# Kernel tuning notes

Hardware: AMD Instinct MI355X
Metric: run time of the kernel (lower is better)

## Reference

```python
import jax, jax.numpy as jnp
import numpy as np


def setup_inputs() -> dict:
    key = jax.random.key(0)
    # [N, n, m]: batch, transform length (axis 1), columns
    x = jax.random.normal(key, (32, 1024, 512), dtype=jnp.float32)
    return {"x": x}


def reference(x):
    # Faithful port of idct_odd_case: IDCT-III via a length-2n complex IFFT
    # on a Hermitian-symmetric-style mirrored array, exactly as the TF code.
    N, n, m = x.shape
    k = jnp.arange(n, dtype=jnp.float32)
    # t[k] = sqrt(2n) * exp(i*pi*k/(2n)); t[0] scaled by extra sqrt(2)
    t = jnp.sqrt(2.0 * n) * jnp.exp(1j * k * (np.pi / (2.0 * n)))
    t = t.at[0].multiply(jnp.sqrt(2.0))
    W = t.astype(jnp.complex64)[None, :, None]           # [1, n, 1]
    xc = x.astype(jnp.complex64)
    yy_up = W * xc                                        # [N, n, m]
    # -i * W[1:n] * reverse(x[1:n]) along the transform axis
    yy_down = (-1j) * W[:, 1:, :] * xc[:, n - 1:0:-1, :]  # [N, n-1, m]
    yy_mid = jnp.zeros((N, 1, m), dtype=jnp.complex64)
    yy = jnp.concatenate([yy_up, yy_mid, yy_down], axis=1)  # [N, 2n, m]
    y = jnp.fft.ifft(yy, axis=1)                          # matlab_ifft: ifft on axis 1
    return jnp.real(y[:, :n, :]).astype(jnp.float32)
```

## Files before the change

### kernel.cpp

```cpp
#include <hip/hip_runtime.h>

typedef unsigned short u16;
typedef __attribute__((ext_vector_type(8))) __bf16 bf16x8;
typedef __attribute__((ext_vector_type(4))) float f32x4;

#define GLOAD_LDS16(g, l)                                                                     \
  __builtin_amdgcn_global_load_lds((const __attribute__((address_space(1))) unsigned int*)(g), \
                                   (__attribute__((address_space(3))) unsigned int*)(l), 16, 0, 0)

static __device__ __forceinline__ u16 f2bf(float f) {
  unsigned int u = __float_as_uint(f);
  u += 0x7fffu + ((u >> 16) & 1u);
  return (u16)(u >> 16);
}

#define BATCH 32
#define NN 1024
#define MM 512
#define KH 512

__global__ void fill_eo(u16* __restrict__ E, u16* __restrict__ O) {
  int idx = blockIdx.x * 256 + threadIdx.x;
  int j = idx >> 9;
  int p = idx & 511;
  int tj = 2 * j + 1;
  float ve;
  if (p == 0) {
    ve = 0.03125f;
  } else {
    int pe = (2 * p * tj) & 4095;
    ve = 0.04419417382415922f * cosf((float)pe * 1.5339807878856412e-3f);
  }
  int po = ((2 * p + 1) * tj) & 4095;
  float vo = 0.04419417382415922f * cosf((float)po * 1.5339807878856412e-3f);
  E[idx] = f2bf(ve);
  O[idx] = f2bf(vo);
}

__global__ void conv_t(const float* __restrict__ x, u16* __restrict__ xe,
                       u16* __restrict__ xo) {
  __shared__ u16 tile[32][34];
  const int b = blockIdx.z;
  const int k0 = blockIdx.y << 5;
  const int c0 = blockIdx.x << 5;
  const int t = threadIdx.x;
  {
    const int r = t >> 3;
    const int c4 = (t & 7) << 2;
    const float4 v = *(const float4*)(x + ((size_t)b * NN + k0 + r) * MM + c0 + c4);
    tile[c4 + 0][r] = f2bf(v.x);
    tile[c4 + 1][r] = f2bf(v.y);
    tile[c4 + 2][r] = f2bf(v.z);
    tile[c4 + 3][r] = f2bf(v.w);
  }
  __syncthreads();
  {
    const int c = t >> 3;
    const int ko = (t & 7) << 2;
    const int p0 = (k0 + ko) >> 1;
    ushort2 e, o;
    e.x = tile[c][ko + 0]; e.y = tile[c][ko + 2];
    o.x = tile[c][ko + 1]; o.y = tile[c][ko + 3];
    const size_t rb = ((size_t)b * MM + c0 + c) * KH + p0;
    *(ushort2*)(xe + rb) = e;
    *(ushort2*)(xo + rb) = o;
  }
}

__global__ __launch_bounds__(256, 2) void gemm_idct(const u16* __restrict__ E,
                                                    const u16* __restrict__ O,
                                                    const u16* __restrict__ Xe,
                                                    const u16* __restrict__ Xo,
                                                    float* __restrict__ C) {
  __shared__ __align__(16) u16 sE[128 * 64];
  __shared__ __align__(16) u16 sO[128 * 64];
  __shared__ __align__(16) u16 sXe[128 * 64];
  __shared__ __align__(16) u16 sXo[128 * 64];
  const int wg   = blockIdx.x;
  const int xcd  = wg & 7;
  const int slot = wg >> 3;
  const int tm   = slot & 3;
  const int pair = ((slot >> 2) << 3) | xcd;
  const int tn   = pair & 3;
  const int b    = pair >> 2;

  const int t = threadIdx.x;
  const int wave = t >> 6, lane = t & 63;
  const int wr = wave >> 1, wc = wave & 1;
  const int lhi = lane >> 4, llo = lane & 15;

  const int srow = t >> 3;
  const int sdc  = (t & 7) ^ (srow & 7);

  const u16* gE  = E  + (size_t)(tm * 128 + srow) * KH + sdc * 8;
  const u16* gO  = O  + (size_t)(tm * 128 + srow) * KH + sdc * 8;
  const u16* gXe = Xe + ((size_t)b * MM + tn * 128 + srow) * KH + sdc * 8;
  const u16* gXo = Xo + ((size_t)b * MM + tn * 128 + srow) * KH + sdc * 8;

  f32x4 accE[4][4] = {};
  f32x4 accO[4][4] = {};

  for (int kt = 0; kt < KH; kt += 64) {
#pragma unroll
    for (int c = 0; c < 4; ++c) {
      GLOAD_LDS16(gE  + kt + (size_t)(c * 32) * KH, &sE[c * 2048 + t * 8]);
      GLOAD_LDS16(gO  + kt + (size_t)(c * 32) * KH, &sO[c * 2048 + t * 8]);
      GLOAD_LDS16(gXe + kt + (size_t)(c * 32) * KH, &sXe[c * 2048 + t * 8]);
      GLOAD_LDS16(gXo + kt + (size_t)(c * 32) * KH, &sXo[c * 2048 + t * 8]);
    }
    __syncthreads();

    bf16x8 fe[4][2], fo[4][2], fxe[4][2], fxo[4][2];
#pragma unroll
    for (int i = 0; i < 4; ++i)
#pragma unroll
      for (int ks = 0; ks < 2; ++ks) {
        const int ra = wr * 64 + i * 16 + llo;
        const int rb = wc * 64 + i * 16 + llo;
        const int ca = ((((ks << 2) | lhi)) ^ (llo & 7)) << 3;
        fe[i][ks]  = *(const bf16x8*)&sE[ra * 64 + ca];
        fo[i][ks]  = *(const bf16x8*)&sO[ra * 64 + ca];
        fxe[i][ks] = *(const bf16x8*)&sXe[rb * 64 + ca];
        fxo[i][ks] = *(const bf16x8*)&sXo[rb * 64 + ca];
      }
#pragma unroll
    for (int ks = 0; ks < 2; ++ks) {
#pragma unroll
      for (int mi = 0; mi < 4; ++mi)
#pragma unroll
        for (int ni = 0; ni < 4; ++ni)
          accE[mi][ni] = __builtin_amdgcn_mfma_f32_16x16x32_bf16(
              fe[mi][ks], fxe[ni][ks], accE[mi][ni], 0, 0, 0);
#pragma unroll
      for (int mi = 0; mi < 4; ++mi)
#pragma unroll
        for (int ni = 0; ni < 4; ++ni)
          accO[mi][ni] = __builtin_amdgcn_mfma_f32_16x16x32_bf16(
              fo[mi][ks], fxo[ni][ks], accO[mi][ni], 0, 0, 0);
    }
    __syncthreads();
  }

  float* Cb = C + (size_t)b * NN * MM;
  const int jhbase = tm * 128 + wr * 64 + lhi * 4;
  const int cbase  = tn * 128 + wc * 64 + llo;
#pragma unroll
  for (int mi = 0; mi < 4; ++mi)
#pragma unroll
    for (int ni = 0; ni < 4; ++ni) {
      const int jh = jhbase + mi * 16;
      const int c  = cbase + ni * 16;
#pragma unroll
      for (int r = 0; r < 4; ++r) {
        const float ye = accE[mi][ni][r];
        const float yo = accO[mi][ni][r];
        Cb[(size_t)(jh + r) * MM + c]            = ye + yo;
        Cb[(size_t)(NN - 1 - (jh + r)) * MM + c] = ye - yo;
      }
    }
}

extern "C" void kernel_launch(void* const* d_in, const int* in_sizes, int n_in,
                              void* d_out, int out_size, void* d_ws, size_t ws_size,
                              hipStream_t stream) {
  const float* x = (const float*)d_in[0];
  float* out = (float*)d_out;
  u16* E  = (u16*)d_ws;
  u16* O  = E + (size_t)KH * KH;
  u16* xe = O + (size_t)KH * KH;
  u16* xo = xe + (size_t)BATCH * MM * KH;

  fill_eo<<<dim3((KH * KH) / 256), dim3(256), 0, stream>>>(E, O);
  conv_t<<<dim3(MM / 32, NN / 32, BATCH), dim3(256), 0, stream>>>(x, xe, xo);
  gemm_idct<<<dim3(512), dim3(256), 0, stream>>>(E, O, xe, xo, out);
}
```

Before: 50.26 us.

## Fuse fp32-to-bf16 transpose into GEMM and double-buffer pre-swizzled basis loads

Removes the separate conv_t kernel. The GEMM now loads fp32 x directly into registers, converts it to bf16 and writes even/odd interleaved, swizzled tiles into LDS. The E/O cosine matrices are merged into one pre-swizzled G matrix that is double-buffered through LDS with async global-to-LDS loads, overlapping the next stage's loads with the MFMAs. Occupancy is raised to 3 waves per SIMD. The intent is to drop the intermediate bf16 write and read of x and one kernel launch, at the cost of more register pressure and in-loop conversion work.

```diff
diff --git a/kernel.cpp b/kernel.cpp
--- a/kernel.cpp
+++ b/kernel.cpp
@@ -19,63 +19,34 @@
 #define MM 512
 #define KH 512
 
-__global__ void fill_eo(u16* __restrict__ E, u16* __restrict__ O) {
+static __device__ __forceinline__ int swz(int r) { return ((r >> 1) ^ ((r & 1) << 2)) & 7; }
+
+__global__ void fill_g(u16* __restrict__ G) {
   int idx = blockIdx.x * 256 + threadIdx.x;
-  int j = idx >> 9;
-  int p = idx & 511;
-  int tj = 2 * j + 1;
-  float ve;
-  if (p == 0) {
-    ve = 0.03125f;
+  int j = idx >> 10;
+  int r = idx & 1023;
+  int s = r >> 6;
+  int cp = (r >> 3) & 7;
+  int sub = r & 7;
+  int chunk = cp ^ swz(j);
+  int k;
+  if (chunk < 4) k = 2 * (s * 32 + chunk * 8 + sub);
+  else           k = 2 * (s * 32 + (chunk - 4) * 8 + sub) + 1;
+  float v;
+  if (k == 0) {
+    v = 0.03125f;
   } else {
-    int pe = (2 * p * tj) & 4095;
-    ve = 0.04419417382415922f * cosf((float)pe * 1.5339807878856412e-3f);
+    int ph = (k * (2 * j + 1)) & 4095;
+    v = 0.04419417382415922f * cosf((float)ph * 1.5339807878856412e-3f);
   }
-  int po = ((2 * p + 1) * tj) & 4095;
-  float vo = 0.04419417382415922f * cosf((float)po * 1.5339807878856412e-3f);
-  E[idx] = f2bf(ve);
-  O[idx] = f2bf(vo);
+  G[idx] = f2bf(v);
 }
 
-__global__ void conv_t(const float* __restrict__ x, u16* __restrict__ xe,
-                       u16* __restrict__ xo) {
-  __shared__ u16 tile[32][34];
-  const int b = blockIdx.z;
-  const int k0 = blockIdx.y << 5;
-  const int c0 = blockIdx.x << 5;
-  const int t = threadIdx.x;
-  {
-    const int r = t >> 3;
-    const int c4 = (t & 7) << 2;
-    const float4 v = *(const float4*)(x + ((size_t)b * NN + k0 + r) * MM + c0 + c4);
-    tile[c4 + 0][r] = f2bf(v.x);
-    tile[c4 + 1][r] = f2bf(v.y);
-    tile[c4 + 2][r] = f2bf(v.z);
-    tile[c4 + 3][r] = f2bf(v.w);
-  }
-  __syncthreads();
-  {
-    const int c = t >> 3;
-    const int ko = (t & 7) << 2;
-    const int p0 = (k0 + ko) >> 1;
-    ushort2 e, o;
-    e.x = tile[c][ko + 0]; e.y = tile[c][ko + 2];
-    o.x = tile[c][ko + 1]; o.y = tile[c][ko + 3];
-    const size_t rb = ((size_t)b * MM + c0 + c) * KH + p0;
-    *(ushort2*)(xe + rb) = e;
-    *(ushort2*)(xo + rb) = o;
-  }
-}
-
-__global__ __launch_bounds__(256, 2) void gemm_idct(const u16* __restrict__ E,
-                                                    const u16* __restrict__ O,
-                                                    const u16* __restrict__ Xe,
-                                                    const u16* __restrict__ Xo,
+__global__ __launch_bounds__(256, 3) void gemm_idct(const u16* __restrict__ G,
+                                                    const float* __restrict__ X,
                                                     float* __restrict__ C) {
-  __shared__ __align__(16) u16 sE[128 * 64];
-  __shared__ __align__(16) u16 sO[128 * 64];
-  __shared__ __align__(16) u16 sXe[128 * 64];
-  __shared__ __align__(16) u16 sXo[128 * 64];
+  __shared__ __align__(16) u16 sA[2][128 * 64];
+  __shared__ __align__(16) u16 sX[128 * 64];
   const int wg   = blockIdx.x;
   const int xcd  = wg & 7;
   const int slot = wg >> 3;
@@ -89,55 +60,79 @@
   const int wr = wave >> 1, wc = wave & 1;
   const int lhi = lane >> 4, llo = lane & 15;
 
-  const int srow = t >> 3;
-  const int sdc  = (t & 7) ^ (srow & 7);
+  const u16* srcA = G + ((size_t)(tm * 128 + (t >> 3)) << 10) + (t & 7) * 8;
+#define ISSUE_A(s)                                                             \
+  do {                                                                         \
+    u16* dst = &sA[(s) & 1][0];                                                \
+    _Pragma("unroll") for (int c = 0; c < 4; ++c)                              \
+      GLOAD_LDS16(srcA + c * 32768 + (s) * 64, dst + c * 2048 + t * 8);        \
+  } while (0)
 
-  const u16* gE  = E  + (size_t)(tm * 128 + srow) * KH + sdc * 8;
-  const u16* gO  = O  + (size_t)(tm * 128 + srow) * KH + sdc * 8;
-  const u16* gXe = Xe + ((size_t)b * MM + tn * 128 + srow) * KH + sdc * 8;
-  const u16* gXo = Xo + ((size_t)b * MM + tn * 128 + srow) * KH + sdc * 8;
+  const int cp2 = (t & 63) << 1;
+  const int kq  = t >> 6;
+  const float* gX = X + ((size_t)b * NN + kq * 16) * MM + tn * 128 + cp2;
+
+  float2 xr[16];
+#define LOAD_X(s)                                                              \
+  do {                                                                         \
+    const float* p = gX + (size_t)(s) * 64 * MM;                               \
+    _Pragma("unroll") for (int i = 0; i < 16; ++i)                             \
+      xr[i] = *(const float2*)(p + (size_t)i * MM);                            \
+  } while (0)
+
+#define WRITE_X()                                                              \
+  do {                                                                         \
+    _Pragma("unroll") for (int cc = 0; cc < 2; ++cc) {                         \
+      const int c = cp2 + cc;                                                  \
+      const int fc = swz(c);                                                   \
+      bf16x8 e, o;                                                             \
+      _Pragma("unroll") for (int m = 0; m < 8; ++m) {                          \
+        e[m] = (__bf16)(cc ? xr[2 * m].y : xr[2 * m].x);                       \
+        o[m] = (__bf16)(cc ? xr[2 * m + 1].y : xr[2 * m + 1].x);               \
+      }                                                                        \
+      *(bf16x8*)&sX[c * 64 + ((kq ^ fc) << 3)] = e;                            \
+      *(bf16x8*)&sX[c * 64 + (((4 + kq) ^ fc) << 3)] = o;                      \
+    }                                                                          \
+  } while (0)
 
   f32x4 accE[4][4] = {};
   f32x4 accO[4][4] = {};
 
-  for (int kt = 0; kt < KH; kt += 64) {
+  ISSUE_A(0);
+  LOAD_X(0);
+  __syncthreads();
+
+  for (int s = 0; s < 16; ++s) {
+    WRITE_X();
+    __syncthreads();
+    if (s < 15) {
+      ISSUE_A(s + 1);
+      LOAD_X(s + 1);
+    }
+    const u16* lA = &sA[s & 1][0];
+    bf16x8 fe[4], fo[4], fxe[4], fxo[4];
 #pragma unroll
-    for (int c = 0; c < 4; ++c) {
-      GLOAD_LDS16(gE  + kt + (size_t)(c * 32) * KH, &sE[c * 2048 + t * 8]);
-      GLOAD_LDS16(gO  + kt + (size_t)(c * 32) * KH, &sO[c * 2048 + t * 8]);
-      GLOAD_LDS16(gXe + kt + (size_t)(c * 32) * KH, &sXe[c * 2048 + t * 8]);
-      GLOAD_LDS16(gXo + kt + (size_t)(c * 32) * KH, &sXo[c * 2048 + t * 8]);
+    for (int i = 0; i < 4; ++i) {
+      const int ra = wr * 64 + i * 16 + llo;
+      const int rb = wc * 64 + i * 16 + llo;
+      const int fa = swz(ra), fb = swz(rb);
+      fe[i]  = *(const bf16x8*)&lA[ra * 64 + ((lhi ^ fa) << 3)];
+      fo[i]  = *(const bf16x8*)&lA[ra * 64 + (((4 + lhi) ^ fa) << 3)];
+      fxe[i] = *(const bf16x8*)&sX[rb * 64 + ((lhi ^ fb) << 3)];
+      fxo[i] = *(const bf16x8*)&sX[rb * 64 + (((4 + lhi) ^ fb) << 3)];
     }
-    __syncthreads();
-
-    bf16x8 fe[4][2], fo[4][2], fxe[4][2], fxo[4][2];
 #pragma unroll
-    for (int i = 0; i < 4; ++i)
+    for (int mi = 0; mi < 4; ++mi)
 #pragma unroll
-      for (int ks = 0; ks < 2; ++ks) {
-        const int ra = wr * 64 + i * 16 + llo;
-        const int rb = wc * 64 + i * 16 + llo;
-        const int ca = ((((ks << 2) | lhi)) ^ (llo & 7)) << 3;
-        fe[i][ks]  = *(const bf16x8*)&sE[ra * 64 + ca];
-        fo[i][ks]  = *(const bf16x8*)&sO[ra * 64 + ca];
-        fxe[i][ks] = *(const bf16x8*)&sXe[rb * 64 + ca];
-        fxo[i][ks] = *(const bf16x8*)&sXo[rb * 64 + ca];
-      }
+      for (int ni = 0; ni < 4; ++ni)
+        accE[mi][ni] = __builtin_amdgcn_mfma_f32_16x16x32_bf16(
+            fe[mi], fxe[ni], accE[mi][ni], 0, 0, 0);
 #pragma unroll
-    for (int ks = 0; ks < 2; ++ks) {
+    for (int mi = 0; mi < 4; ++mi)
 #pragma unroll
-      for (int mi = 0; mi < 4; ++mi)
-#pragma unroll
-        for (int ni = 0; ni < 4; ++ni)
-          accE[mi][ni] = __builtin_amdgcn_mfma_f32_16x16x32_bf16(
-              fe[mi][ks], fxe[ni][ks], accE[mi][ni], 0, 0, 0);
-#pragma unroll
-      for (int mi = 0; mi < 4; ++mi)
-#pragma unroll
-        for (int ni = 0; ni < 4; ++ni)
-          accO[mi][ni] = __builtin_amdgcn_mfma_f32_16x16x32_bf16(
-              fo[mi][ks], fxo[ni][ks], accO[mi][ni], 0, 0, 0);
-    }
+      for (int ni = 0; ni < 4; ++ni)
+        accO[mi][ni] = __builtin_amdgcn_mfma_f32_16x16x32_bf16(
+            fo[mi], fxo[ni], accO[mi][ni], 0, 0, 0);
     __syncthreads();
   }
 
@@ -158,6 +153,9 @@
         Cb[(size_t)(NN - 1 - (jh + r)) * MM + c] = ye - yo;
       }
     }
+#undef ISSUE_A
+#undef LOAD_X
+#undef WRITE_X
 }
 
 extern "C" void kernel_launch(void* const* d_in, const int* in_sizes, int n_in,
@@ -165,12 +163,8 @@
                               hipStream_t stream) {
   const float* x = (const float*)d_in[0];
   float* out = (float*)d_out;
-  u16* E  = (u16*)d_ws;
-  u16* O  = E + (size_t)KH * KH;
-  u16* xe = O + (size_t)KH * KH;
-  u16* xo = xe + (size_t)BATCH * MM * KH;
+  u16* G = (u16*)d_ws;
 
-  fill_eo<<<dim3((KH * KH) / 256), dim3(256), 0, stream>>>(E, O);
-  conv_t<<<dim3(MM / 32, NN / 32, BATCH), dim3(256), 0, stream>>>(x, xe, xo);
-  gemm_idct<<<dim3(512), dim3(256), 0, stream>>>(E, O, xe, xo, out);
+  fill_g<<<dim3((512 * 1024) / 256), dim3(256), 0, stream>>>(G);
+  gemm_idct<<<dim3(512), dim3(256), 0, stream>>>(G, x, out);
 }
```

Measured after the change: 65.82 us. 30.9% more time.
